# Performance work log

Measured on AMD Instinct MI355X. Metric: run time of the kernel, lower is better.

## Reference

```python
import jax, jax.numpy as jnp
import numpy as np

VOCAB = 32000
D_MODEL = 1024
D_FF = 4 * D_MODEL
N_LAYERS = 2
N_EXPERTS = 8
TOP_K = 2
BATCH = 4
SEQ = 2048
LN_EPS = 1e-5


def setup_inputs() -> dict:
    key = jax.random.key(0)
    ks = jax.random.split(key, 12)
    s = lambda *dims: 1.0 / np.sqrt(dims[-2] if len(dims) > 1 else dims[-1])
    inp = {
        "tokens": jax.random.randint(ks[0], (BATCH, SEQ), 0, VOCAB, dtype=jnp.int32),
        "symbolic_emb": jax.random.normal(ks[1], (BATCH, D_MODEL), dtype=jnp.float32),
        "emb": jax.random.normal(ks[2], (VOCAB, D_MODEL), dtype=jnp.float32) * 0.02,
        "gate_w": jax.random.normal(ks[3], (N_LAYERS, D_MODEL, N_EXPERTS), dtype=jnp.float32) / np.sqrt(D_MODEL),
        "gate_b": jnp.zeros((N_LAYERS, N_EXPERTS), dtype=jnp.float32),
        "w1": jax.random.normal(ks[4], (N_LAYERS, N_EXPERTS, D_MODEL, D_FF), dtype=jnp.float32) / np.sqrt(D_MODEL),
        "b1": jnp.zeros((N_LAYERS, N_EXPERTS, D_FF), dtype=jnp.float32),
        "w2": jax.random.normal(ks[5], (N_LAYERS, N_EXPERTS, D_FF, D_MODEL), dtype=jnp.float32) / np.sqrt(D_FF),
        "b2": jnp.zeros((N_LAYERS, N_EXPERTS, D_MODEL), dtype=jnp.float32),
        "ln_g": jnp.ones((D_MODEL,), dtype=jnp.float32),
        "ln_b": jnp.zeros((D_MODEL,), dtype=jnp.float32),
    }
    return inp


def _moe_layer(x_flat, gw, gb, w1, b1, w2, b2):
    # x_flat: [T, d]
    probs = jax.nn.softmax(x_flat @ gw + gb, axis=-1)            # [T, E]
    weights, idx = jax.lax.top_k(probs, TOP_K)                   # [T, K]
    # combine weight per (token, expert): sum of top-k weights routed to that expert
    combine = jnp.sum(jax.nn.one_hot(idx, N_EXPERTS, dtype=x_flat.dtype) * weights[..., None], axis=1)  # [T, E]
    out = jnp.zeros_like(x_flat)
    for j in range(N_EXPERTS):  # small fixed structural loop
        h = jax.nn.gelu(x_flat @ w1[j] + b1[j], approximate=False)  # [T, d_ff]
        y = h @ w2[j] + b2[j]                                       # [T, d]
        out = out + combine[:, j:j + 1] * y
    return out


def reference(tokens, symbolic_emb, emb, gate_w, gate_b, w1, b1, w2, b2, ln_g, ln_b):
    x = emb[tokens] + symbolic_emb[:, None, :]                  # [B, S, d]
    T = BATCH * SEQ
    x = x.reshape(T, D_MODEL)
    for l in range(N_LAYERS):
        x = _moe_layer(x, gate_w[l], gate_b[l], w1[l], b1[l], w2[l], b2[l])
    mu = jnp.mean(x, axis=-1, keepdims=True)
    var = jnp.mean(jnp.square(x - mu), axis=-1, keepdims=True)
    x = (x - mu) * jax.lax.rsqrt(var + LN_EPS) * ln_g + ln_b
    return x.reshape(BATCH, SEQ, D_MODEL)
```

## Files before the change

kernel.cpp:

```cpp
#include <hip/hip_runtime.h>
#include <math.h>

#define T_TOK 8192
#define DM 1024
#define DFF 4096
#define NE 8
#define NPAIR 16384
#define MT256 72
#define MT128 136
#define LN_EPS 1e-5f

typedef __attribute__((ext_vector_type(8))) short bf16x8;
typedef __attribute__((ext_vector_type(4))) float f32x4;
typedef __attribute__((ext_vector_type(4))) unsigned short u16x4;
typedef __attribute__((ext_vector_type(8))) unsigned short u16x8;
typedef unsigned int u32;
typedef unsigned short u16;

__device__ __forceinline__ u16 f2bf(float f) {
  union { float f; u32 u; } v; v.f = f;
  u32 r = (v.u + 0x7fffu + ((v.u >> 16) & 1u)) >> 16;
  return (u16)r;
}
__device__ __forceinline__ float bf2f(u16 h) {
  union { u32 u; float f; } v; v.u = ((u32)h) << 16; return v.f;
}
__device__ __forceinline__ float gelu_exact(float v) {
  return 0.5f * v * (1.0f + erff(v * 0.70710678118654752f));
}
__device__ __forceinline__ float gelu_fast(float v) {
  float u = v * (0.7978845608f + 0.0356774081f * v * v);
  float t = __expf(-2.0f * fabsf(u));
  float th = (1.0f - t) / (1.0f + t);
  th = copysignf(th, u);
  return 0.5f * v * (1.0f + th);
}

__device__ __forceinline__ void gll16(const void* g, void* l) {
  __builtin_amdgcn_global_load_lds(
      (const __attribute__((address_space(1))) u32*)g,
      (__attribute__((address_space(3))) u32*)l, 16, 0, 0);
}

__global__ __launch_bounds__(256) void embed_kernel(const int* __restrict__ tok,
    const float* __restrict__ sym, const float* __restrict__ emb,
    float* __restrict__ x, u16* __restrict__ xh, u16* __restrict__ xl)
{
  int t = blockIdx.x;
  int b = t >> 11;
  int tk = tok[t];
  int d = threadIdx.x * 4;
  f32x4 e = *(const f32x4*)(emb + (size_t)tk * DM + d);
  f32x4 s = *(const f32x4*)(sym + (size_t)b * DM + d);
  f32x4 v = e + s;
  *(f32x4*)(x + (size_t)t * DM + d) = v;
  u16x4 hv, lv;
#pragma unroll
  for (int j = 0; j < 4; ++j) {
    u16 hb = f2bf(v[j]);
    hv[j] = hb;
    lv[j] = f2bf(v[j] - bf2f(hb));
  }
  *(u16x4*)(xh + (size_t)t * DM + d) = hv;
  *(u16x4*)(xl + (size_t)t * DM + d) = lv;
}

__global__ __launch_bounds__(256) void gate_kernel(const float* __restrict__ x,
    const float* __restrict__ gw, const float* __restrict__ gb,
    int* __restrict__ topk_idx, float* __restrict__ topk_w)
{
  int lane = threadIdx.x & 63;
  int t = blockIdx.x * 4 + (threadIdx.x >> 6);
  const float* xr = x + (size_t)t * DM;
  double a[8] = {0,0,0,0,0,0,0,0};
  for (int i = 0; i < 16; ++i) {
    int d = i * 64 + lane;
    double xv = (double)xr[d];
    const float* g = gw + (size_t)d * NE;
#pragma unroll
    for (int j = 0; j < 8; ++j) a[j] += xv * (double)g[j];
  }
#pragma unroll
  for (int j = 0; j < 8; ++j) {
#pragma unroll
    for (int sh = 32; sh; sh >>= 1) a[j] += __shfl_xor(a[j], sh);
  }
  if (lane == 0) {
#pragma unroll
    for (int j = 0; j < 8; ++j) a[j] += (double)gb[j];
    double m = a[0];
    for (int j = 1; j < 8; ++j) m = a[j] > m ? a[j] : m;
    double p[8], sum = 0.0;
    for (int j = 0; j < 8; ++j) { p[j] = exp(a[j] - m); sum += p[j]; }
    for (int j = 0; j < 8; ++j) p[j] /= sum;
    int j0 = 0; double b0 = p[0];
    for (int j = 1; j < 8; ++j) if (p[j] > b0) { b0 = p[j]; j0 = j; }
    int j1 = (j0 == 0) ? 1 : 0; double b1v = p[j1];
    for (int j = 0; j < 8; ++j) if (j != j0 && p[j] > b1v) { b1v = p[j]; j1 = j; }
    topk_idx[t*2]   = j0; topk_idx[t*2+1] = j1;
    topk_w[t*2]     = (float)b0; topk_w[t*2+1] = (float)b1v;
  }
}

__global__ __launch_bounds__(256) void count_kernel(const int* __restrict__ topk_idx,
    int* __restrict__ meta)
{
  __shared__ int hist[8];
  int tid = threadIdx.x;
  if (tid < 8) hist[tid] = 0;
  __syncthreads();
  int t = blockIdx.x * 256 + tid;
  atomicAdd(&hist[topk_idx[t*2] & 7], 1);
  atomicAdd(&hist[topk_idx[t*2+1] & 7], 1);
  __syncthreads();
  if (tid < 8) meta[256 + blockIdx.x * 8 + tid] = hist[tid];
}

__global__ __launch_bounds__(64) void scan_kernel(int* __restrict__ meta)
{
  __shared__ int tot[8], off[9], tb2[8], tb1[8];
  int lane = threadIdx.x;
  if (lane < 8) {
    int s = 0;
    for (int b = 0; b < 32; ++b) s += meta[256 + b * 8 + lane];
    tot[lane] = s;
  }
  __syncthreads();
  if (lane == 0) {
    int s = 0, n2 = 0, n1 = 0;
    for (int e = 0; e < 8; ++e) {
      off[e] = s; s += tot[e];
      tb2[e] = n2; n2 += (tot[e] + 255) >> 8;
      tb1[e] = n1; n1 += (tot[e] + 127) >> 7;
    }
    off[8] = s;
    for (int i = n2; i < MT256; ++i) meta[32 + i] = -1;
    for (int i = n1; i < MT128; ++i) meta[104 + i] = -1;
  }
  __syncthreads();
  if (lane < 9) meta[8 + lane] = off[lane];
  if (lane < 8) {
    meta[lane] = tot[lane];
    int n2 = (tot[lane] + 255) >> 8;
    for (int i = 0; i < n2; ++i) meta[32 + tb2[lane] + i] = (lane << 16) | i;
    int n1 = (tot[lane] + 127) >> 7;
    for (int i = 0; i < n1; ++i) meta[104 + tb1[lane] + i] = (lane << 16) | i;
    int run = off[lane];
    for (int b = 0; b < 32; ++b) {
      meta[512 + b * 8 + lane] = run;
      run += meta[256 + b * 8 + lane];
    }
  }
}

__global__ __launch_bounds__(256) void scatter_kernel(int* __restrict__ topk_idx,
    const int* __restrict__ meta, int* __restrict__ pair_token)
{
  __shared__ int hist[8];
  __shared__ int base[8];
  int tid = threadIdx.x;
  if (tid < 8) { hist[tid] = 0; base[tid] = meta[512 + blockIdx.x * 8 + tid]; }
  __syncthreads();
  int t = blockIdx.x * 256 + tid;
#pragma unroll
  for (int k = 0; k < 2; ++k) {
    int e = topk_idx[t*2 + k] & 7;
    int pos = atomicAdd(&hist[e], 1);
    int slot = base[e] + pos;
    pair_token[slot] = t;
    topk_idx[t*2 + k] = e | (slot << 3);
  }
}

template<bool LO>
__global__ __launch_bounds__(256) void transpose_kernel(const float* __restrict__ src,
    u16* __restrict__ dsth, u16* __restrict__ dstl, int K, int N)
{
  __shared__ float tile[64][65];
  int e = blockIdx.z;
  const float* s = src + (size_t)e * K * N;
  size_t dbase = (size_t)e * K * N;
  int n0 = blockIdx.x * 64, k0 = blockIdx.y * 64;
  int tid = threadIdx.x;
#pragma unroll
  for (int j = 0; j < 4; ++j) {
    int kl = j * 16 + (tid >> 4);
    int nn = (tid & 15) * 4;
    f32x4 v = *(const f32x4*)(s + (size_t)(k0 + kl) * N + n0 + nn);
    tile[nn + 0][kl] = v.x;
    tile[nn + 1][kl] = v.y;
    tile[nn + 2][kl] = v.z;
    tile[nn + 3][kl] = v.w;
  }
  __syncthreads();
#pragma unroll
  for (int it = 0; it < 2; ++it) {
    int task = it * 256 + tid;
    int nr = task >> 3;
    int ch = task & 7;
    u16x8 oh, ol;
#pragma unroll
    for (int j = 0; j < 8; ++j) {
      float v = tile[nr][ch*8 + j];
      u16 hb = f2bf(v);
      oh[j] = hb;
      if (LO) ol[j] = f2bf(v - bf2f(hb));
    }
    size_t doff = dbase + (size_t)(n0 + nr) * K + k0 + ch*8;
    *(u16x8*)(dsth + doff) = oh;
    if (LO) *(u16x8*)(dstl + doff) = ol;
  }
}

__global__ __launch_bounds__(256) void w2g_kernel(const float* __restrict__ w2,
    const float* __restrict__ gw, float* __restrict__ w2g)
{
  int wid = blockIdx.x * 4 + (threadIdx.x >> 6);
  int lane = threadIdx.x & 63;
  int e = wid >> 12, f = wid & 4095;
  const float* row = w2 + ((size_t)e * DFF + f) * DM;
  float a0=0,a1=0,a2=0,a3=0,a4=0,a5=0,a6=0,a7=0;
  for (int i = 0; i < 4; ++i) {
    int d0 = i * 256 + lane * 4;
    f32x4 xv = *(const f32x4*)(row + d0);
#pragma unroll
    for (int q = 0; q < 4; ++q) {
      const f32x4* gr = (const f32x4*)(gw + (size_t)(d0 + q) * 8);
      f32x4 g0 = gr[0], g1 = gr[1];
      float xq = xv[q];
      a0 += xq*g0.x; a1 += xq*g0.y; a2 += xq*g0.z; a3 += xq*g0.w;
      a4 += xq*g1.x; a5 += xq*g1.y; a6 += xq*g1.z; a7 += xq*g1.w;
    }
  }
  float acc[8] = {a0,a1,a2,a3,a4,a5,a6,a7};
#pragma unroll
  for (int j = 0; j < 8; ++j) {
#pragma unroll
    for (int sh = 32; sh; sh >>= 1) acc[j] += __shfl_xor(acc[j], sh);
  }
  if (lane == 0) {
#pragma unroll
    for (int j = 0; j < 8; ++j) w2g[(size_t)wid * 8 + j] = acc[j];
  }
}

__global__ __launch_bounds__(256) void b2g_kernel(const float* __restrict__ b2,
    const float* __restrict__ gw, float* __restrict__ b2g)
{
  int w = blockIdx.x * 4 + (threadIdx.x >> 6);
  int lane = threadIdx.x & 63;
  int e = w >> 3, j = w & 7;
  float acc = 0.f;
  for (int i = 0; i < 16; ++i) {
    int d = i * 64 + lane;
    acc += b2[(size_t)e * DM + d] * gw[(size_t)d * 8 + j];
  }
#pragma unroll
  for (int sh = 32; sh; sh >>= 1) acc += __shfl_xor(acc, sh);
  if (lane == 0) b2g[w] = acc;
}

__global__ __launch_bounds__(256) void reducer_kernel(const float* __restrict__ Rp,
    float* __restrict__ R)
{
  int i = blockIdx.x * 256 + threadIdx.x;
  float s = 0.f;
#pragma unroll
  for (int nt = 0; nt < 16; ++nt) s += Rp[(size_t)nt * NPAIR * 8 + i];
  R[i] = s;
}

__global__ __launch_bounds__(256) void gate1_kernel(const float* __restrict__ R,
    const float* __restrict__ b2g, const float* __restrict__ gb,
    int* __restrict__ topk_idx, float* __restrict__ topk_w)
{
  int t = blockIdx.x * 256 + threadIdx.x;
  int v0 = topk_idx[t*2], v1 = topk_idx[t*2+1];
  int e0 = v0 & 7, e1 = v1 & 7;
  int s0 = v0 >> 3, s1 = v1 >> 3;
  double w0 = (double)topk_w[t*2], w1 = (double)topk_w[t*2+1];
  double a[8];
#pragma unroll
  for (int j = 0; j < 8; ++j)
    a[j] = w0 * ((double)R[(size_t)s0*8+j] + (double)b2g[e0*8+j])
         + w1 * ((double)R[(size_t)s1*8+j] + (double)b2g[e1*8+j])
         + (double)gb[j];
  double m = a[0];
  for (int j = 1; j < 8; ++j) m = a[j] > m ? a[j] : m;
  double p[8], sum = 0.0;
  for (int j = 0; j < 8; ++j) { p[j] = exp(a[j] - m); sum += p[j]; }
  for (int j = 0; j < 8; ++j) p[j] /= sum;
  int j0 = 0; double b0 = p[0];
  for (int j = 1; j < 8; ++j) if (p[j] > b0) { b0 = p[j]; j0 = j; }
  int j1 = (j0 == 0) ? 1 : 0; double b1v = p[j1];
  for (int j = 0; j < 8; ++j) if (j != j0 && p[j] > b1v) { b1v = p[j]; j1 = j; }
  topk_idx[t*2]   = j0; topk_idx[t*2+1] = j1;
  topk_w[t*2]     = (float)b0; topk_w[t*2+1] = (float)b1v;
}

template<int K0, int NSEG, int NTOT, bool GATHER, int MODE>
__global__ __launch_bounds__(512, 2) void gemm256_kernel(
    const u16* __restrict__ Ah, const u16* __restrict__ Al,
    const u16* __restrict__ Bh, const u16* __restrict__ Bl,
    const float* __restrict__ bias, const int* __restrict__ off,
    const int* __restrict__ tiletab, const int* __restrict__ pair_token,
    u16* __restrict__ outh, const float* __restrict__ W2G,
    float* __restrict__ Rpart)
{
  constexpr int NT = (K0 * NSEG) / 64;
  static_assert(NT >= 2, "");
  const int tt = tiletab[blockIdx.y];
  if (tt < 0) return;
  const int e  = tt >> 16;
  const int mt = tt & 0xffff;
  const int off_e = off[e], off_e1 = off[e + 1];
  const int p0 = off_e + mt * 256;
  const int NX = gridDim.x;
  int bx = blockIdx.x;
  int ntile = ((NX & 7) == 0) ? ((bx & 7) * (NX >> 3) + (bx >> 3)) : bx;
  const int n0 = ntile * 256;

  __shared__ __align__(16) u16 ALs[2][2][8192];
  __shared__ __align__(16) u16 BLs[2][2][8192];

  const int tid  = threadIdx.x;
  const int lane = tid & 63;
  const int wave = tid >> 6;
  const int wm = wave >> 2;
  const int wn = wave & 3;
  const int wbase = tid & 448;

  size_t aoff[2], boff[2];
#pragma unroll
  for (int i = 0; i < 2; ++i) {
    int c = i * 512 + tid;
    int r = c >> 2;
    int cs = (c & 3) ^ ((r >> 1) & 3);
    int idx = p0 + r;
    if (idx >= off_e1) idx = p0;
    int ar = GATHER ? pair_token[idx] : idx;
    aoff[i] = (size_t)ar * K0 + (size_t)(cs * 8);
    boff[i] = ((size_t)e * NTOT + n0 + r) * K0 + (size_t)(cs * 8);
  }

  auto stageA = [&](int t, int kh) {
    int kk = t * 64 + kh * 32;
    int seg = (NSEG == 3) ? (kk >> 10) : 0;
    int kc  = (NSEG == 3) ? (kk & (K0 - 1)) : kk;
    const u16* base = (NSEG == 3 && seg == 1) ? Al : Ah;
    u16* dst = &ALs[t & 1][kh][0];
#pragma unroll
    for (int i = 0; i < 2; ++i)
      gll16(base + aoff[i] + kc, dst + (i * 512 + wbase) * 8);
  };
  auto stageB = [&](int t, int kh) {
    int kk = t * 64 + kh * 32;
    int seg = (NSEG == 3) ? (kk >> 10) : 0;
    int kc  = (NSEG == 3) ? (kk & (K0 - 1)) : kk;
    const u16* base = (NSEG == 3 && seg == 2) ? Bl : Bh;
    u16* dst = &BLs[t & 1][kh][0];
#pragma unroll
    for (int i = 0; i < 2; ++i)
      gll16(base + boff[i] + kc, dst + (i * 512 + wbase) * 8);
  };

  f32x4 acc[8][4];
  const f32x4 fzero = {0.f, 0.f, 0.f, 0.f};
#pragma unroll
  for (int m = 0; m < 8; ++m)
#pragma unroll
    for (int n = 0; n < 4; ++n) acc[m][n] = fzero;

  auto rdA4 = [&](bf16x8* dst, int par, int kh, int mbase) {
    const u16* L = &ALs[par][kh][0];
#pragma unroll
    for (int mf = 0; mf < 4; ++mf) {
      int row = wm * 128 + (mbase + mf) * 16 + (lane & 15);
      dst[mf] = *(const bf16x8*)&L[row * 32 + (((lane >> 4) ^ ((row >> 1) & 3)) << 3)];
    }
  };
  auto rdB4 = [&](bf16x8* dst, int par, int kh) {
    const u16* L = &BLs[par][kh][0];
#pragma unroll
    for (int nf = 0; nf < 4; ++nf) {
      int row = wn * 64 + nf * 16 + (lane & 15);
      dst[nf] = *(const bf16x8*)&L[row * 32 + (((lane >> 4) ^ ((row >> 1) & 3)) << 3)];
    }
  };

#define MMBLK(MB, A4, B4)                                                        \
  {                                                                              \
    __builtin_amdgcn_s_setprio(1);                                               \
    _Pragma("unroll")                                                            \
    for (int mf = 0; mf < 4; ++mf)                                               \
      _Pragma("unroll")                                                          \
      for (int nf = 0; nf < 4; ++nf)                                             \
        acc[(MB) + mf][nf] = __builtin_amdgcn_mfma_f32_16x16x32_bf16(            \
            (A4)[mf], (B4)[nf], acc[(MB) + mf][nf], 0, 0, 0);                    \
    __builtin_amdgcn_s_setprio(0);                                               \
  }

  stageA(0, 0); stageB(0, 0);
  stageA(0, 1); stageB(0, 1);
  stageA(1, 0); stageB(1, 0);
  asm volatile("s_waitcnt vmcnt(8)" ::: "memory");
  __builtin_amdgcn_s_barrier();
  asm volatile("" ::: "memory");

  for (int t = 0; t < NT; ++t) {
    const int par = t & 1;
    bf16x8 bA[4], aA[4], aB[4], bC[4], aC[4], aD[4];
    rdB4(bA, par, 0);
    rdA4(aA, par, 0, 0);
    if (t + 1 < NT) stageA(t + 1, 1);
    __builtin_amdgcn_s_barrier();
    MMBLK(0, aA, bA);
    __builtin_amdgcn_s_barrier();
    rdA4(aB, par, 0, 4);
    if (t + 1 < NT) stageB(t + 1, 1);
    __builtin_amdgcn_s_barrier();
    MMBLK(4, aB, bA);
    if (t + 1 < NT) { asm volatile("s_waitcnt vmcnt(8)" ::: "memory"); }
    else            { asm volatile("s_waitcnt vmcnt(0)" ::: "memory"); }
    __builtin_amdgcn_s_barrier();
    asm volatile("" ::: "memory");
    rdB4(bC, par, 1);
    rdA4(aC, par, 1, 0);
    if (t + 2 < NT) stageA(t + 2, 0);
    __builtin_amdgcn_s_barrier();
    MMBLK(0, aC, bC);
    __builtin_amdgcn_s_barrier();
    rdA4(aD, par, 1, 4);
    if (t + 2 < NT) stageB(t + 2, 0);
    __builtin_amdgcn_s_barrier();
    MMBLK(4, aD, bC);
    if (t + 1 < NT) {
      if (t + 2 < NT) { asm volatile("s_waitcnt vmcnt(8)" ::: "memory"); }
      else            { asm volatile("s_waitcnt vmcnt(4)" ::: "memory"); }
      __builtin_amdgcn_s_barrier();
      asm volatile("" ::: "memory");
    }
  }
#undef MMBLK

  float bv[4];
#pragma unroll
  for (int nf = 0; nf < 4; ++nf)
    bv[nf] = bias[(size_t)e * NTOT + n0 + wn * 64 + nf * 16 + (lane & 15)];

  if constexpr (MODE == 3) {
    __syncthreads();
    float* Rpt = (float*)&ALs[0][0][0];
    f32x4 wg0[4], wg1[4];
#pragma unroll
    for (int nf = 0; nf < 4; ++nf) {
      int col = n0 + wn * 64 + nf * 16 + (lane & 15);
      const float* wp = W2G + ((size_t)e * NTOT + col) * 8;
      wg0[nf] = *(const f32x4*)wp;
      wg1[nf] = *(const f32x4*)(wp + 4);
    }
#pragma unroll
    for (int mf = 0; mf < 8; ++mf) {
      f32x4 pr0[4], pr1[4];
#pragma unroll
      for (int r = 0; r < 4; ++r) { pr0[r] = fzero; pr1[r] = fzero; }
      int rbase = p0 + wm * 128 + mf * 16 + ((lane >> 4) << 2);
#pragma unroll
      for (int nf = 0; nf < 4; ++nf) {
        int col = n0 + wn * 64 + nf * 16 + (lane & 15);
#pragma unroll
        for (int r = 0; r < 4; ++r) {
          float v = gelu_exact(acc[mf][nf][r] + bv[nf]);
          if (rbase + r < off_e1)
            outh[(size_t)(rbase + r) * NTOT + col] = f2bf(v);
          pr0[r] += v * wg0[nf];
          pr1[r] += v * wg1[nf];
        }
      }
#pragma unroll
      for (int r = 0; r < 4; ++r) {
#pragma unroll
        for (int sh = 1; sh < 16; sh <<= 1) {
#pragma unroll
          for (int q = 0; q < 4; ++q) {
            pr0[r][q] += __shfl_xor(pr0[r][q], sh);
            pr1[r][q] += __shfl_xor(pr1[r][q], sh);
          }
        }
        if ((lane & 15) == 0) {
          int rl = wm * 128 + mf * 16 + ((lane >> 4) << 2) + r;
          float* dst = Rpt + ((size_t)(wn * 256 + rl)) * 8;
          *(f32x4*)dst = pr0[r];
          *(f32x4*)(dst + 4) = pr1[r];
        }
      }
    }
    __syncthreads();
    for (int i = tid; i < 256 * 8; i += 512) {
      int rl = i >> 3, j = i & 7;
      float ssum = Rpt[(size_t)(0 * 256 + rl) * 8 + j]
                 + Rpt[(size_t)(1 * 256 + rl) * 8 + j]
                 + Rpt[(size_t)(2 * 256 + rl) * 8 + j]
                 + Rpt[(size_t)(3 * 256 + rl) * 8 + j];
      int p = p0 + rl;
      if (p < off_e1)
        Rpart[((size_t)ntile * NPAIR + p) * 8 + j] = ssum;
    }
  } else {
#pragma unroll
    for (int mf = 0; mf < 8; ++mf) {
      int rbase = p0 + wm * 128 + mf * 16 + ((lane >> 4) << 2);
#pragma unroll
      for (int nf = 0; nf < 4; ++nf) {
        int col = n0 + wn * 64 + nf * 16 + (lane & 15);
#pragma unroll
        for (int r = 0; r < 4; ++r) {
          if (rbase + r < off_e1) {
            float v = gelu_fast(acc[mf][nf][r] + bv[nf]);
            outh[(size_t)(rbase + r) * NTOT + col] = f2bf(v);
          }
        }
      }
    }
  }
}

template<int K0, int NTOT, bool GATHER>
__global__ __launch_bounds__(256, 4) void gemm128_kernel(
    const u16* __restrict__ Ah, const u16* __restrict__ Bh,
    const float* __restrict__ bias, const int* __restrict__ off,
    const int* __restrict__ tiletab, const int* __restrict__ pair_token,
    float* __restrict__ outy)
{
  constexpr int NT = K0 / 32;
  const int tt = tiletab[blockIdx.y];
  if (tt < 0) return;
  const int e  = tt >> 16;
  const int mt = tt & 0xffff;
  const int off_e = off[e], off_e1 = off[e + 1];
  const int p0 = off_e + mt * 128;
  const int NX = gridDim.x;
  int bx = blockIdx.x;
  int ntile = ((NX & 7) == 0) ? ((bx & 7) * (NX >> 3) + (bx >> 3)) : bx;
  const int n0 = ntile * 128;

  __shared__ __align__(16) u16 AL[2][4096];
  __shared__ __align__(16) u16 BL[2][4096];

  const int tid  = threadIdx.x;
  const int lane = tid & 63;
  const int wave = tid >> 6;
  const int wm = wave >> 1, wn = wave & 1;
  const int wbase = tid & 192;

  size_t aoff[2], boff[2];
#pragma unroll
  for (int i = 0; i < 2; ++i) {
    int c = i * 256 + tid;
    int r = c >> 2;
    int cs = (c & 3) ^ ((r >> 1) & 3);
    int idx = p0 + r;
    if (idx >= off_e1) idx = p0;
    int ar = GATHER ? pair_token[idx] : idx;
    aoff[i] = (size_t)ar * K0 + (size_t)(cs * 8);
    boff[i] = ((size_t)e * NTOT + n0 + r) * K0 + (size_t)(cs * 8);
  }

  auto stage = [&](int b, int t) {
    int kc = t * 32;
#pragma unroll
    for (int i = 0; i < 2; ++i) {
      int cb = i * 256 + wbase;
      gll16(Ah + aoff[i] + kc, &AL[b][cb * 8]);
      gll16(Bh + boff[i] + kc, &BL[b][cb * 8]);
    }
  };

  f32x4 acc[4][4];
  const f32x4 fzero = {0.f, 0.f, 0.f, 0.f};
#pragma unroll
  for (int m = 0; m < 4; ++m)
#pragma unroll
    for (int n = 0; n < 4; ++n) acc[m][n] = fzero;

  stage(0, 0);
  __syncthreads();

  int buf = 0;
  for (int t = 0; t < NT; ++t) {
    if (t + 1 < NT) stage(buf ^ 1, t + 1);
    bf16x8 af[4], bf[4];
#pragma unroll
    for (int m = 0; m < 4; ++m) {
      int row = wm * 64 + m * 16 + (lane & 15);
      af[m] = *(const bf16x8*)&AL[buf][row * 32 + (((lane >> 4) ^ ((row >> 1) & 3)) << 3)];
    }
#pragma unroll
    for (int n = 0; n < 4; ++n) {
      int row = wn * 64 + n * 16 + (lane & 15);
      bf[n] = *(const bf16x8*)&BL[buf][row * 32 + (((lane >> 4) ^ ((row >> 1) & 3)) << 3)];
    }
    __builtin_amdgcn_s_setprio(1);
#pragma unroll
    for (int m = 0; m < 4; ++m)
#pragma unroll
      for (int n = 0; n < 4; ++n)
        acc[m][n] = __builtin_amdgcn_mfma_f32_16x16x32_bf16(af[m], bf[n], acc[m][n], 0, 0, 0);
    __builtin_amdgcn_s_setprio(0);
    __syncthreads();
    buf ^= 1;
  }

  float bv[4];
#pragma unroll
  for (int n = 0; n < 4; ++n)
    bv[n] = bias[(size_t)e * NTOT + n0 + wn * 64 + n * 16 + (lane & 15)];

#pragma unroll
  for (int m = 0; m < 4; ++m) {
    int rbase = p0 + wm * 64 + m * 16 + ((lane >> 4) << 2);
#pragma unroll
    for (int n = 0; n < 4; ++n) {
      int col = n0 + wn * 64 + n * 16 + (lane & 15);
#pragma unroll
      for (int r = 0; r < 4; ++r) {
        int rowp = rbase + r;
        if (rowp < off_e1)
          outy[(size_t)rowp * NTOT + col] = acc[m][n][r] + bv[n];
      }
    }
  }
}

__global__ __launch_bounds__(256) void combine0_kernel(const float* __restrict__ y,
    const int* __restrict__ topk_idx, const float* __restrict__ topk_w,
    u16* __restrict__ xh)
{
  int t = blockIdx.x;
  int d = threadIdx.x * 4;
  int s0 = topk_idx[t*2] >> 3, s1 = topk_idx[t*2 + 1] >> 3;
  float w0 = topk_w[t*2], w1 = topk_w[t*2 + 1];
  f32x4 y0 = *(const f32x4*)(y + (size_t)s0 * DM + d);
  f32x4 y1 = *(const f32x4*)(y + (size_t)s1 * DM + d);
  f32x4 v = y0 * w0 + y1 * w1;
  u16x4 hv;
#pragma unroll
  for (int j = 0; j < 4; ++j) hv[j] = f2bf(v[j]);
  *(u16x4*)(xh + (size_t)t * DM + d) = hv;
}

__global__ __launch_bounds__(256) void combine1_ln_kernel(const float* __restrict__ y,
    const int* __restrict__ topk_idx, const float* __restrict__ topk_w,
    const float* __restrict__ g, const float* __restrict__ b, float* __restrict__ out)
{
  int t = blockIdx.x;
  int d = threadIdx.x * 4;
  int s0 = topk_idx[t*2] >> 3, s1 = topk_idx[t*2 + 1] >> 3;
  float w0 = topk_w[t*2], w1 = topk_w[t*2 + 1];
  f32x4 y0 = *(const f32x4*)(y + (size_t)s0 * DM + d);
  f32x4 y1 = *(const f32x4*)(y + (size_t)s1 * DM + d);
  f32x4 v = y0 * w0 + y1 * w1;
  float s = v.x + v.y + v.z + v.w;
  float sq = v.x*v.x + v.y*v.y + v.z*v.z + v.w*v.w;
#pragma unroll
  for (int sh = 32; sh; sh >>= 1) { s += __shfl_xor(s, sh); sq += __shfl_xor(sq, sh); }
  __shared__ float red[8];
  int wave = threadIdx.x >> 6, lane = threadIdx.x & 63;
  if (lane == 0) { red[wave] = s; red[4 + wave] = sq; }
  __syncthreads();
  s = red[0] + red[1] + red[2] + red[3];
  sq = red[4] + red[5] + red[6] + red[7];
  float mu = s * (1.0f / DM);
  float var = sq * (1.0f / DM) - mu * mu;
  float inv = rsqrtf(var + LN_EPS);
  f32x4 gv = *(const f32x4*)(g + d);
  f32x4 bv = *(const f32x4*)(b + d);
  f32x4 o;
  o.x = (v.x - mu) * inv * gv.x + bv.x;
  o.y = (v.y - mu) * inv * gv.y + bv.y;
  o.z = (v.z - mu) * inv * gv.z + bv.z;
  o.w = (v.w - mu) * inv * gv.w + bv.w;
  *(f32x4*)(out + (size_t)t * DM + d) = o;
}

extern "C" void kernel_launch(void* const* d_in, const int* in_sizes, int n_in,
                              void* d_out, int out_size, void* d_ws, size_t ws_size,
                              hipStream_t stream)
{
  const int*   tokens = (const int*)d_in[0];
  const float* sym    = (const float*)d_in[1];
  const float* emb    = (const float*)d_in[2];
  const float* gate_w = (const float*)d_in[3];
  const float* gate_b = (const float*)d_in[4];
  const float* w1     = (const float*)d_in[5];
  const float* b1     = (const float*)d_in[6];
  const float* w2     = (const float*)d_in[7];
  const float* b2     = (const float*)d_in[8];
  const float* ln_g   = (const float*)d_in[9];
  const float* ln_b   = (const float*)d_in[10];

  char* ws = (char*)d_ws;
  float* x   = (float*)(ws);
  u16*   xh  = (u16*)  (ws + 33554432);
  u16*   xl  = (u16*)  (ws + 50331648);
  u16*   hh  = (u16*)  (ws + 67108864);
  float* W2G   = (float*)(ws + 201326592);
  float* Rpart = (float*)(ws + 202375168);
  float* B2G   = (float*)(ws + 219152384);
  float* R     = (float*)(ws + 219152640);
  float* y     = (float*)(ws + 219676928);
  u16*   wTh = (u16*)  (ws + 335544320);
  u16*   wTl = (u16*)  (ws + 402653184);
  int*   pair_token = (int*)  (ws + 469762048);
  int*   topk_idx   = (int*)  (ws + 469893120);
  float* topk_w     = (float*)(ws + 469958656);
  int*   meta       = (int*)  (ws + 470024192);

  embed_kernel<<<T_TOK, 256, 0, stream>>>(tokens, sym, emb, x, xh, xl);

  gate_kernel<<<T_TOK / 4, 256, 0, stream>>>(x, gate_w, gate_b, topk_idx, topk_w);
  count_kernel<<<T_TOK / 256, 256, 0, stream>>>(topk_idx, meta);
  scan_kernel<<<1, 64, 0, stream>>>(meta);
  scatter_kernel<<<T_TOK / 256, 256, 0, stream>>>(topk_idx, meta, pair_token);

  w2g_kernel<<<NE * DFF / 4, 256, 0, stream>>>(w2, gate_w + (size_t)DM * NE, W2G);
  b2g_kernel<<<16, 256, 0, stream>>>(b2, gate_w + (size_t)DM * NE, B2G);

  transpose_kernel<true><<<dim3(DFF / 64, DM / 64, NE), 256, 0, stream>>>(
      w1, wTh, wTl, DM, DFF);
  gemm256_kernel<DM, 3, DFF, true, 3><<<dim3(DFF / 256, MT256), 512, 0, stream>>>(
      xh, xl, wTh, wTl, b1, meta + 8, meta + 32, pair_token, hh, W2G, Rpart);

  reducer_kernel<<<NPAIR * 8 / 256, 256, 0, stream>>>(Rpart, R);

  transpose_kernel<false><<<dim3(DM / 64, DFF / 64, NE), 256, 0, stream>>>(
      w2, wTh, nullptr, DFF, DM);
  gemm128_kernel<DFF, DM, false><<<dim3(DM / 128, MT128), 256, 0, stream>>>(
      hh, wTh, b2, meta + 8, meta + 104, pair_token, y);

  combine0_kernel<<<T_TOK, 256, 0, stream>>>(y, topk_idx, topk_w, xh);

  gate1_kernel<<<T_TOK / 256, 256, 0, stream>>>(R, B2G, gate_b + NE,
                                                topk_idx, topk_w);
  count_kernel<<<T_TOK / 256, 256, 0, stream>>>(topk_idx, meta);
  scan_kernel<<<1, 64, 0, stream>>>(meta);
  scatter_kernel<<<T_TOK / 256, 256, 0, stream>>>(topk_idx, meta, pair_token);

  transpose_kernel<false><<<dim3(DFF / 64, DM / 64, NE), 256, 0, stream>>>(
      w1 + (size_t)NE * DM * DFF, wTh, nullptr, DM, DFF);
  gemm256_kernel<DM, 1, DFF, true, 0><<<dim3(DFF / 256, MT256), 512, 0, stream>>>(
      xh, nullptr, wTh, nullptr, b1 + (size_t)NE * DFF, meta + 8, meta + 32,
      pair_token, hh, nullptr, nullptr);

  transpose_kernel<false><<<dim3(DM / 64, DFF / 64, NE), 256, 0, stream>>>(
      w2 + (size_t)NE * DFF * DM, wTh, nullptr, DFF, DM);
  gemm128_kernel<DFF, DM, false><<<dim3(DM / 128, MT128), 256, 0, stream>>>(
      hh, wTh, b2 + (size_t)NE * DM, meta + 8, meta + 104, pair_token, y);

  combine1_ln_kernel<<<T_TOK, 256, 0, stream>>>(y, topk_idx, topk_w,
                                                ln_g, ln_b, (float*)d_out);
}
```

Measured before the change: 1.617 ms.

## Fuse embed with gating, store expert outputs as bf16, use 128-tile GEMM for layer-1 up-projection

Merges the embedding and layer-0 gate into one kernel, so the fp32 activation buffer is no longer written and re-read. The down-projection GEMMs now write their outputs in bf16 instead of fp32, and the combine kernels read bf16, roughly halving that traffic. The layer-1 up-projection moves from the 256-tile GEMM to the 128-tile GEMM with a fused fast-GELU epilogue, and the 256 kernel keeps only the router-fused mode. The cost is reduced precision in the expert outputs, and the layer-1 up-projection may run less efficiently with the smaller tiles.

```diff
diff --git a/kernel.cpp b/kernel.cpp
--- a/kernel.cpp
+++ b/kernel.cpp
@@ -42,9 +42,11 @@
       (__attribute__((address_space(3))) u32*)l, 16, 0, 0);
 }
 
-__global__ __launch_bounds__(256) void embed_kernel(const int* __restrict__ tok,
+__global__ __launch_bounds__(256) void embed_gate_kernel(const int* __restrict__ tok,
     const float* __restrict__ sym, const float* __restrict__ emb,
-    float* __restrict__ x, u16* __restrict__ xh, u16* __restrict__ xl)
+    const float* __restrict__ gw, const float* __restrict__ gb,
+    u16* __restrict__ xh, u16* __restrict__ xl,
+    int* __restrict__ topk_idx, float* __restrict__ topk_w)
 {
   int t = blockIdx.x;
   int b = t >> 11;
@@ -53,7 +55,6 @@
   f32x4 e = *(const f32x4*)(emb + (size_t)tk * DM + d);
   f32x4 s = *(const f32x4*)(sym + (size_t)b * DM + d);
   f32x4 v = e + s;
-  *(f32x4*)(x + (size_t)t * DM + d) = v;
   u16x4 hv, lv;
 #pragma unroll
   for (int j = 0; j < 4; ++j) {
@@ -63,35 +64,39 @@
   }
   *(u16x4*)(xh + (size_t)t * DM + d) = hv;
   *(u16x4*)(xl + (size_t)t * DM + d) = lv;
-}
-
-__global__ __launch_bounds__(256) void gate_kernel(const float* __restrict__ x,
-    const float* __restrict__ gw, const float* __restrict__ gb,
-    int* __restrict__ topk_idx, float* __restrict__ topk_w)
-{
-  int lane = threadIdx.x & 63;
-  int t = blockIdx.x * 4 + (threadIdx.x >> 6);
-  const float* xr = x + (size_t)t * DM;
+
   double a[8] = {0,0,0,0,0,0,0,0};
-  for (int i = 0; i < 16; ++i) {
-    int d = i * 64 + lane;
-    double xv = (double)xr[d];
-    const float* g = gw + (size_t)d * NE;
-#pragma unroll
-    for (int j = 0; j < 8; ++j) a[j] += xv * (double)g[j];
+#pragma unroll
+  for (int q = 0; q < 4; ++q) {
+    const f32x4* gr = (const f32x4*)(gw + (size_t)(d + q) * 8);
+    f32x4 g0 = gr[0], g1 = gr[1];
+    double xv = (double)v[q];
+    a[0] += xv*(double)g0.x; a[1] += xv*(double)g0.y;
+    a[2] += xv*(double)g0.z; a[3] += xv*(double)g0.w;
+    a[4] += xv*(double)g1.x; a[5] += xv*(double)g1.y;
+    a[6] += xv*(double)g1.z; a[7] += xv*(double)g1.w;
   }
 #pragma unroll
   for (int j = 0; j < 8; ++j) {
 #pragma unroll
     for (int sh = 32; sh; sh >>= 1) a[j] += __shfl_xor(a[j], sh);
   }
+  __shared__ double red[4][8];
+  int wave = threadIdx.x >> 6, lane = threadIdx.x & 63;
   if (lane == 0) {
 #pragma unroll
-    for (int j = 0; j < 8; ++j) a[j] += (double)gb[j];
-    double m = a[0];
-    for (int j = 1; j < 8; ++j) m = a[j] > m ? a[j] : m;
+    for (int j = 0; j < 8; ++j) red[wave][j] = a[j];
+  }
+  __syncthreads();
+  if (threadIdx.x == 0) {
+    double lg[8];
+#pragma unroll
+    for (int j = 0; j < 8; ++j)
+      lg[j] = red[0][j] + red[1][j] + red[2][j] + red[3][j] + (double)gb[j];
+    double m = lg[0];
+    for (int j = 1; j < 8; ++j) m = lg[j] > m ? lg[j] : m;
     double p[8], sum = 0.0;
-    for (int j = 0; j < 8; ++j) { p[j] = exp(a[j] - m); sum += p[j]; }
+    for (int j = 0; j < 8; ++j) { p[j] = exp(lg[j] - m); sum += p[j]; }
     for (int j = 0; j < 8; ++j) p[j] /= sum;
     int j0 = 0; double b0 = p[0];
     for (int j = 1; j < 8; ++j) if (p[j] > b0) { b0 = p[j]; j0 = j; }
@@ -298,7 +303,7 @@
   topk_w[t*2]     = (float)b0; topk_w[t*2+1] = (float)b1v;
 }
 
-template<int K0, int NSEG, int NTOT, bool GATHER, int MODE>
+template<int K0, int NSEG, int NTOT, bool GATHER>
 __global__ __launch_bounds__(512, 2) void gemm256_kernel(
     const u16* __restrict__ Ah, const u16* __restrict__ Al,
     const u16* __restrict__ Bh, const u16* __restrict__ Bl,
@@ -448,89 +453,71 @@
   for (int nf = 0; nf < 4; ++nf)
     bv[nf] = bias[(size_t)e * NTOT + n0 + wn * 64 + nf * 16 + (lane & 15)];
 
-  if constexpr (MODE == 3) {
-    __syncthreads();
-    float* Rpt = (float*)&ALs[0][0][0];
-    f32x4 wg0[4], wg1[4];
+  __syncthreads();
+  float* Rpt = (float*)&ALs[0][0][0];
+  f32x4 wg0[4], wg1[4];
+#pragma unroll
+  for (int nf = 0; nf < 4; ++nf) {
+    int col = n0 + wn * 64 + nf * 16 + (lane & 15);
+    const float* wp = W2G + ((size_t)e * NTOT + col) * 8;
+    wg0[nf] = *(const f32x4*)wp;
+    wg1[nf] = *(const f32x4*)(wp + 4);
+  }
+#pragma unroll
+  for (int mf = 0; mf < 8; ++mf) {
+    f32x4 pr0[4], pr1[4];
+#pragma unroll
+    for (int r = 0; r < 4; ++r) { pr0[r] = fzero; pr1[r] = fzero; }
+    int rbase = p0 + wm * 128 + mf * 16 + ((lane >> 4) << 2);
 #pragma unroll
     for (int nf = 0; nf < 4; ++nf) {
       int col = n0 + wn * 64 + nf * 16 + (lane & 15);
-      const float* wp = W2G + ((size_t)e * NTOT + col) * 8;
-      wg0[nf] = *(const f32x4*)wp;
-      wg1[nf] = *(const f32x4*)(wp + 4);
-    }
-#pragma unroll
-    for (int mf = 0; mf < 8; ++mf) {
-      f32x4 pr0[4], pr1[4];
-#pragma unroll
-      for (int r = 0; r < 4; ++r) { pr0[r] = fzero; pr1[r] = fzero; }
-      int rbase = p0 + wm * 128 + mf * 16 + ((lane >> 4) << 2);
-#pragma unroll
-      for (int nf = 0; nf < 4; ++nf) {
-        int col = n0 + wn * 64 + nf * 16 + (lane & 15);
-#pragma unroll
-        for (int r = 0; r < 4; ++r) {
-          float v = gelu_exact(acc[mf][nf][r] + bv[nf]);
-          if (rbase + r < off_e1)
-            outh[(size_t)(rbase + r) * NTOT + col] = f2bf(v);
-          pr0[r] += v * wg0[nf];
-          pr1[r] += v * wg1[nf];
+#pragma unroll
+      for (int r = 0; r < 4; ++r) {
+        float v = gelu_exact(acc[mf][nf][r] + bv[nf]);
+        if (rbase + r < off_e1)
+          outh[(size_t)(rbase + r) * NTOT + col] = f2bf(v);
+        pr0[r] += v * wg0[nf];
+        pr1[r] += v * wg1[nf];
+      }
+    }
+#pragma unroll
+    for (int r = 0; r < 4; ++r) {
+#pragma unroll
+      for (int sh = 1; sh < 16; sh <<= 1) {
+#pragma unroll
+        for (int q = 0; q < 4; ++q) {
+          pr0[r][q] += __shfl_xor(pr0[r][q], sh);
+          pr1[r][q] += __shfl_xor(pr1[r][q], sh);
         }
       }
-#pragma unroll
-      for (int r = 0; r < 4; ++r) {
-#pragma unroll
-        for (int sh = 1; sh < 16; sh <<= 1) {
-#pragma unroll
-          for (int q = 0; q < 4; ++q) {
-            pr0[r][q] += __shfl_xor(pr0[r][q], sh);
-            pr1[r][q] += __shfl_xor(pr1[r][q], sh);
-          }
-        }
-        if ((lane & 15) == 0) {
-          int rl = wm * 128 + mf * 16 + ((lane >> 4) << 2) + r;
-          float* dst = Rpt + ((size_t)(wn * 256 + rl)) * 8;
-          *(f32x4*)dst = pr0[r];
-          *(f32x4*)(dst + 4) = pr1[r];
-        }
+      if ((lane & 15) == 0) {
+        int rl = wm * 128 + mf * 16 + ((lane >> 4) << 2) + r;
+        float* dst = Rpt + ((size_t)(wn * 256 + rl)) * 8;
+        *(f32x4*)dst = pr0[r];
+        *(f32x4*)(dst + 4) = pr1[r];
       }
     }
-    __syncthreads();
-    for (int i = tid; i < 256 * 8; i += 512) {
-      int rl = i >> 3, j = i & 7;
-      float ssum = Rpt[(size_t)(0 * 256 + rl) * 8 + j]
-                 + Rpt[(size_t)(1 * 256 + rl) * 8 + j]
-                 + Rpt[(size_t)(2 * 256 + rl) * 8 + j]
-                 + Rpt[(size_t)(3 * 256 + rl) * 8 + j];
-      int p = p0 + rl;
-      if (p < off_e1)
-        Rpart[((size_t)ntile * NPAIR + p) * 8 + j] = ssum;
-    }
-  } else {
-#pragma unroll
-    for (int mf = 0; mf < 8; ++mf) {
-      int rbase = p0 + wm * 128 + mf * 16 + ((lane >> 4) << 2);
-#pragma unroll
-      for (int nf = 0; nf < 4; ++nf) {
-        int col = n0 + wn * 64 + nf * 16 + (lane & 15);
-#pragma unroll
-        for (int r = 0; r < 4; ++r) {
-          if (rbase + r < off_e1) {
-            float v = gelu_fast(acc[mf][nf][r] + bv[nf]);
-            outh[(size_t)(rbase + r) * NTOT + col] = f2bf(v);
-          }
-        }
-      }
-    }
-  }
-}
-
-template<int K0, int NTOT, bool GATHER>
+  }
+  __syncthreads();
+  for (int i = tid; i < 256 * 8; i += 512) {
+    int rl = i >> 3, j = i & 7;
+    float ssum = Rpt[(size_t)(0 * 256 + rl) * 8 + j]
+               + Rpt[(size_t)(1 * 256 + rl) * 8 + j]
+               + Rpt[(size_t)(2 * 256 + rl) * 8 + j]
+               + Rpt[(size_t)(3 * 256 + rl) * 8 + j];
+    int p = p0 + rl;
+    if (p < off_e1)
+      Rpart[((size_t)ntile * NPAIR + p) * 8 + j] = ssum;
+  }
+}
+
+template<int K0, int NTOT, bool GATHER, int MODE>
 __global__ __launch_bounds__(256, 4) void gemm128_kernel(
     const u16* __restrict__ Ah, const u16* __restrict__ Bh,
     const float* __restrict__ bias, const int* __restrict__ off,
     const int* __restrict__ tiletab, const int* __restrict__ pair_token,
-    float* __restrict__ outy)
+    u16* __restrict__ outp)
 {
   constexpr int NT = K0 / 32;
   const int tt = tiletab[blockIdx.y];
@@ -625,14 +612,17 @@
 #pragma unroll
       for (int r = 0; r < 4; ++r) {
         int rowp = rbase + r;
-        if (rowp < off_e1)
-          outy[(size_t)rowp * NTOT + col] = acc[m][n][r] + bv[n];
+        if (rowp < off_e1) {
+          float v = acc[m][n][r] + bv[n];
+          if constexpr (MODE == 0) v = gelu_fast(v);
+          outp[(size_t)rowp * NTOT + col] = f2bf(v);
+        }
       }
     }
   }
 }
 
-__global__ __launch_bounds__(256) void combine0_kernel(const float* __restrict__ y,
+__global__ __launch_bounds__(256) void combine0_kernel(const u16* __restrict__ yb,
     const int* __restrict__ topk_idx, const float* __restrict__ topk_w,
     u16* __restrict__ xh)
 {
@@ -640,16 +630,16 @@
   int d = threadIdx.x * 4;
   int s0 = topk_idx[t*2] >> 3, s1 = topk_idx[t*2 + 1] >> 3;
   float w0 = topk_w[t*2], w1 = topk_w[t*2 + 1];
-  f32x4 y0 = *(const f32x4*)(y + (size_t)s0 * DM + d);
-  f32x4 y1 = *(const f32x4*)(y + (size_t)s1 * DM + d);
-  f32x4 v = y0 * w0 + y1 * w1;
+  u16x4 y0 = *(const u16x4*)(yb + (size_t)s0 * DM + d);
+  u16x4 y1 = *(const u16x4*)(yb + (size_t)s1 * DM + d);
   u16x4 hv;
 #pragma unroll
-  for (int j = 0; j < 4; ++j) hv[j] = f2bf(v[j]);
+  for (int j = 0; j < 4; ++j)
+    hv[j] = f2bf(bf2f(y0[j]) * w0 + bf2f(y1[j]) * w1);
   *(u16x4*)(xh + (size_t)t * DM + d) = hv;
 }
 
-__global__ __launch_bounds__(256) void combine1_ln_kernel(const float* __restrict__ y,
+__global__ __launch_bounds__(256) void combine1_ln_kernel(const u16* __restrict__ yb,
     const int* __restrict__ topk_idx, const float* __restrict__ topk_w,
     const float* __restrict__ g, const float* __restrict__ b, float* __restrict__ out)
 {
@@ -657,9 +647,12 @@
   int d = threadIdx.x * 4;
   int s0 = topk_idx[t*2] >> 3, s1 = topk_idx[t*2 + 1] >> 3;
   float w0 = topk_w[t*2], w1 = topk_w[t*2 + 1];
-  f32x4 y0 = *(const f32x4*)(y + (size_t)s0 * DM + d);
-  f32x4 y1 = *(const f32x4*)(y + (size_t)s1 * DM + d);
-  f32x4 v = y0 * w0 + y1 * w1;
+  u16x4 y0 = *(const u16x4*)(yb + (size_t)s0 * DM + d);
+  u16x4 y1 = *(const u16x4*)(yb + (size_t)s1 * DM + d);
+  f32x4 v;
+#pragma unroll
+  for (int j = 0; j < 4; ++j)
+    v[j] = bf2f(y0[j]) * w0 + bf2f(y1[j]) * w1;
   float s = v.x + v.y + v.z + v.w;
   float sq = v.x*v.x + v.y*v.y + v.z*v.z + v.w*v.w;
 #pragma unroll
@@ -700,7 +693,7 @@
   const float* ln_b   = (const float*)d_in[10];
 
   char* ws = (char*)d_ws;
-  float* x   = (float*)(ws);
+  u16*   yb  = (u16*)  (ws);
   u16*   xh  = (u16*)  (ws + 33554432);
   u16*   xl  = (u16*)  (ws + 50331648);
   u16*   hh  = (u16*)  (ws + 67108864);
@@ -708,7 +701,6 @@
   float* Rpart = (float*)(ws + 202375168);
   float* B2G   = (float*)(ws + 219152384);
   float* R     = (float*)(ws + 219152640);
-  float* y     = (float*)(ws + 219676928);
   u16*   wTh = (u16*)  (ws + 335544320);
   u16*   wTl = (u16*)  (ws + 402653184);
   int*   pair_token = (int*)  (ws + 469762048);
@@ -716,9 +708,8 @@
   float* topk_w     = (float*)(ws + 469958656);
   int*   meta       = (int*)  (ws + 470024192);
 
-  embed_kernel<<<T_TOK, 256, 0, stream>>>(tokens, sym, emb, x, xh, xl);
-
-  gate_kernel<<<T_TOK / 4, 256, 0, stream>>>(x, gate_w, gate_b, topk_idx, topk_w);
+  embed_gate_kernel<<<T_TOK, 256, 0, stream>>>(tokens, sym, emb, gate_w, gate_b,
+                                               xh, xl, topk_idx, topk_w);
   count_kernel<<<T_TOK / 256, 256, 0, stream>>>(topk_idx, meta);
   scan_kernel<<<1, 64, 0, stream>>>(meta);
   scatter_kernel<<<T_TOK / 256, 256, 0, stream>>>(topk_idx, meta, pair_token);
@@ -728,17 +719,17 @@
 
   transpose_kernel<true><<<dim3(DFF / 64, DM / 64, NE), 256, 0, stream>>>(
       w1, wTh, wTl, DM, DFF);
-  gemm256_kernel<DM, 3, DFF, true, 3><<<dim3(DFF / 256, MT256), 512, 0, stream>>>(
+  gemm256_kernel<DM, 3, DFF, true><<<dim3(DFF / 256, MT256), 512, 0, stream>>>(
       xh, xl, wTh, wTl, b1, meta + 8, meta + 32, pair_token, hh, W2G, Rpart);
 
   reducer_kernel<<<NPAIR * 8 / 256, 256, 0, stream>>>(Rpart, R);
 
   transpose_kernel<false><<<dim3(DM / 64, DFF / 64, NE), 256, 0, stream>>>(
       w2, wTh, nullptr, DFF, DM);
-  gemm128_kernel<DFF, DM, false><<<dim3(DM / 128, MT128), 256, 0, stream>>>(
-      hh, wTh, b2, meta + 8, meta + 104, pair_token, y);
-
-  combine0_kernel<<<T_TOK, 256, 0, stream>>>(y, topk_idx, topk_w, xh);
+  gemm128_kernel<DFF, DM, false, 2><<<dim3(DM / 128, MT128), 256, 0, stream>>>(
+      hh, wTh, b2, meta + 8, meta + 104, pair_token, yb);
+
+  combine0_kernel<<<T_TOK, 256, 0, stream>>>(yb, topk_idx, topk_w, xh);
 
   gate1_kernel<<<T_TOK / 256, 256, 0, stream>>>(R, B2G, gate_b + NE,
                                                 topk_idx, topk_w);
@@ -748,15 +739,14 @@
 
   transpose_kernel<false><<<dim3(DFF / 64, DM / 64, NE), 256, 0, stream>>>(
       w1 + (size_t)NE * DM * DFF, wTh, nullptr, DM, DFF);
-  gemm256_kernel<DM, 1, DFF, true, 0><<<dim3(DFF / 256, MT256), 512, 0, stream>>>(
-      xh, nullptr, wTh, nullptr, b1 + (size_t)NE * DFF, meta + 8, meta + 32,
-      pair_token, hh, nullptr, nullptr);
+  gemm128_kernel<DM, DFF, true, 0><<<dim3(DFF / 128, MT128), 256, 0, stream>>>(
+      xh, wTh, b1 + (size_t)NE * DFF, meta + 8, meta + 104, pair_token, hh);
 
   transpose_kernel<false><<<dim3(DM / 64, DFF / 64, NE), 256, 0, stream>>>(
       w2 + (size_t)NE * DFF * DM, wTh, nullptr, DFF, DM);
-  gemm128_kernel<DFF, DM, false><<<dim3(DM / 128, MT128), 256, 0, stream>>>(
-      hh, wTh, b2 + (size_t)NE * DM, meta + 8, meta + 104, pair_token, y);
-
-  combine1_ln_kernel<<<T_TOK, 256, 0, stream>>>(y, topk_idx, topk_w,
+  gemm128_kernel<DFF, DM, false, 2><<<dim3(DM / 128, MT128), 256, 0, stream>>>(
+      hh, wTh, b2 + (size_t)NE * DM, meta + 8, meta + 104, pair_token, yb);
+
+  combine1_ln_kernel<<<T_TOK, 256, 0, stream>>>(yb, topk_idx, topk_w,
                                                 ln_g, ln_b, (float*)d_out);
 }
```

Result: faster. 1.578 ms (-2.4%).
